# Performance work log

Hardware: AMD Instinct MI355X
Metric: run time of the kernel (lower is better)

The kernel has to match this reference:

```python
import jax, jax.numpy as jnp
import numpy as np

N_NODES = 50000


def rgcn_conv(x, src, dst, edge_type, W, root, bias):
    """PyG RGCNConv: out[i] = x[i] @ root + bias + sum_r mean_{j in N_r(i)} x[j] @ W[r].
    W: [R, F_in, F_out]. Mean aggregation is per-relation (PyG default aggr='mean')."""
    num_rel = W.shape[0]
    n = x.shape[0]
    out = x @ root + bias
    x_src = x[src]  # [E, F_in] gather once
    for r in range(num_rel):  # small fixed relation count
        mask = (edge_type == r)
        msg = jnp.where(mask[:, None], x_src, 0.0) @ W[r]          # [E, F_out]
        s = jax.ops.segment_sum(msg, dst, num_segments=n)           # [N, F_out]
        c = jax.ops.segment_sum(mask.astype(x.dtype), dst, num_segments=n)  # [N]
        out = out + s / jnp.maximum(c, 1.0)[:, None]
    return out


def setup_inputs() -> dict:
    key = jax.random.key(0)
    ks = jax.random.split(key, 10)
    N, E, F_in, F_hid, F_out, R = N_NODES, 800000, 128, 128, 64, 8
    x = jax.random.normal(ks[0], (N, F_in), dtype=jnp.float32)
    edge_index = jax.random.randint(ks[1], (2, E), 0, N, dtype=jnp.int64)
    edge_type = jax.random.randint(ks[2], (E,), 0, R, dtype=jnp.int64)
    s1 = 1.0 / np.sqrt(F_in)
    s2 = 1.0 / np.sqrt(F_hid)
    W1 = jax.random.normal(ks[3], (R, F_in, F_hid), dtype=jnp.float32) * s1
    root1 = jax.random.normal(ks[4], (F_in, F_hid), dtype=jnp.float32) * s1
    b1 = jnp.zeros((F_hid,), dtype=jnp.float32)
    W2 = jax.random.normal(ks[5], (R, F_hid, F_out), dtype=jnp.float32) * s2
    root2 = jax.random.normal(ks[6], (F_hid, F_out), dtype=jnp.float32) * s2
    b2 = jnp.zeros((F_out,), dtype=jnp.float32)
    return {"x": x, "edge_index": edge_index, "edge_type": edge_type,
            "W1": W1, "root1": root1, "b1": b1,
            "W2": W2, "root2": root2, "b2": b2}


def reference(x, edge_index, edge_type, W1, root1, b1, W2, root2, b2):
    src, dst = edge_index[0], edge_index[1]
    h = jax.nn.relu(rgcn_conv(x, src, dst, edge_type, W1, root1, b1))
    out = rgcn_conv(h, src, dst, edge_type, W2, root2, b2)
    return out
```

## Files before the change

kernel.cpp:

```cpp
#include <hip/hip_runtime.h>

#define N_NODES 50000
#define N_EDGES 800000
#define R_REL   8

#define TNBKT   3125
#define TCAP    512
#define SLAB    2048
#define BINBLK  ((N_EDGES + SLAB - 1) / SLAB)

typedef float  f32x4  __attribute__((ext_vector_type(4)));
typedef __bf16 bf16x8 __attribute__((ext_vector_type(8)));

__device__ __forceinline__ unsigned short f2bf(float f) {
    unsigned int u = __float_as_uint(f);
    u = (u + 0x7FFFu + ((u >> 16) & 1u)) >> 16;
    return (unsigned short)u;
}
__device__ __forceinline__ float bflo(unsigned int u) { return __uint_as_float(u << 16); }
__device__ __forceinline__ float bfhi(unsigned int u) { return __uint_as_float(u & 0xFFFF0000u); }

__device__ __forceinline__ void acc16(float* a, uint4 u0, uint4 u1) {
    a[0]  += bflo(u0.x);   a[1]  += bfhi(u0.x);
    a[2]  += bflo(u0.y);   a[3]  += bfhi(u0.y);
    a[4]  += bflo(u0.z);   a[5]  += bfhi(u0.z);
    a[6]  += bflo(u0.w);   a[7]  += bfhi(u0.w);
    a[8]  += bflo(u1.x);   a[9]  += bfhi(u1.x);
    a[10] += bflo(u1.y);   a[11] += bfhi(u1.y);
    a[12] += bflo(u1.z);   a[13] += bfhi(u1.z);
    a[14] += bflo(u1.w);   a[15] += bfhi(u1.w);
}


#define W1_ELEMS (9 * 128 * 128)
#define W2_ELEMS (9 * 64 * 128)
#define N4       (N_NODES * 32)
#define NB_CVT   ((N4 + 255) / 256)
#define NB_PREP  (BINBLK + NB_CVT)

__global__ __launch_bounds__(256) void k_prep(
    const int* __restrict__ src, const int* __restrict__ dst,
    const int* __restrict__ et, int* __restrict__ gcur,
    unsigned* __restrict__ gbin,
    const float* __restrict__ x, unsigned short* __restrict__ xb,
    const float* __restrict__ root1, const float* __restrict__ W1,
    const float* __restrict__ root2, const float* __restrict__ W2,
    unsigned short* __restrict__ Wt1, unsigned short* __restrict__ Wt2)
{
    __shared__ int hist[TNBKT];
    __shared__ int base[TNBKT];
    const int t = threadIdx.x;

    if (blockIdx.x < BINBLK) {
        const int e0 = blockIdx.x * SLAB;
        for (int i = t; i < TNBKT; i += 256) hist[i] = 0;
        __syncthreads();
#pragma unroll
        for (int i = 0; i < SLAB / 256; ++i) {
            int e = e0 + i * 256 + t;
            if (e < N_EDGES) atomicAdd(&hist[dst[e] >> 4], 1);
        }
        __syncthreads();
        for (int i = t; i < TNBKT; i += 256) {
            int h = hist[i];
            base[i] = (h > 0) ? atomicAdd(&gcur[i], h) : 0;
            hist[i] = 0;
        }
        __syncthreads();
#pragma unroll
        for (int i = 0; i < SLAB / 256; ++i) {
            int e = e0 + i * 256 + t;
            if (e < N_EDGES) {
                int d = dst[e];
                int b = d >> 4;
                int sub = atomicAdd(&hist[b], 1);
                int pos = base[b] + sub;
                unsigned rec = ((unsigned)src[e] << 7) | (unsigned)((d & 15) * 8 + et[e]);
                if (pos < TCAP) gbin[(size_t)b * TCAP + pos] = rec;
            }
        }
        return;
    }

    const int idx = (blockIdx.x - BINBLK) * 256 + t;
    if (idx < N4) {
        float4 v = *(const float4*)(x + (size_t)idx * 4);
        ushort4 o;
        o.x = f2bf(v.x); o.y = f2bf(v.y); o.z = f2bf(v.z); o.w = f2bf(v.w);
        *(ushort4*)(xb + (size_t)idx * 4) = o;
    }
    if (idx < W1_ELEMS) {
        int j    = idx & 7;
        int lane = (idx >> 3) & 63;
        int r    = idx >> 9;
        int nb   = r & 7;
        int r2   = r >> 3;
        int kk   = r2 & 3;
        int seg  = r2 >> 2;
        int k = kk * 32 + (lane >> 4) * 8 + j;
        int n = nb * 16 + (lane & 15);
        float v = (seg == 0) ? root1[k * 128 + n] : W1[((seg - 1) * 128 + k) * 128 + n];
        Wt1[idx] = f2bf(v);
    } else if (idx < W1_ELEMS + W2_ELEMS) {
        int i2   = idx - W1_ELEMS;
        int j    = i2 & 7;
        int lane = (i2 >> 3) & 63;
        int r    = i2 >> 9;
        int nb   = r & 3;
        int r2   = r >> 2;
        int kk   = r2 & 3;
        int seg  = r2 >> 2;
        int k = kk * 32 + (lane >> 4) * 8 + j;
        int n = nb * 16 + (lane & 15);
        float v = (seg == 0) ? root2[k * 64 + n] : W2[((seg - 1) * 128 + k) * 64 + n];
        Wt2[i2] = f2bf(v);
    }
}


template <int FOUT, bool RELU, bool OUT_BF16>
__global__ __launch_bounds__(512) void k_fused(
    const unsigned short* __restrict__ xin,
    const unsigned short* __restrict__ WtP,
    const float* __restrict__ bias,
    const int* __restrict__ gcnt,
    const unsigned* __restrict__ gbin,
    unsigned short* __restrict__ outb,
    float* __restrict__ outf)
{
    constexpr int NBt = FOUT / 16;
    __shared__ __align__(16) unsigned short As0[16][136];
    __shared__ __align__(16) unsigned short As[8][16][136];
    __shared__ unsigned short sorted[TCAP + 8];
    __shared__ int dcnt[128];
    __shared__ int kbeg[128];
    __shared__ int kcur[128];

    const int t = threadIdx.x;
    const int node0 = blockIdx.x * 16;

    if (t < 128) { dcnt[t] = 0; kcur[t] = 0; }
    sorted[t] = 0;
    if (t < 8) sorted[TCAP + t] = 0;
    if (t < 128) {
        const int sr = t >> 3;
        const int sp = t & 7;
        const uint4* s4 = (const uint4*)(xin + (size_t)(node0 + sr) * 128 + sp * 16);
        uint4 r0 = s4[0], r1 = s4[1];
        uint4* d = (uint4*)&As0[sr][sp * 16];
        d[0] = r0; d[1] = r1;
    }
    const int nraw = gcnt[blockIdx.x];
    const int n = nraw < TCAP ? nraw : TCAP;
    unsigned rec = 0;
    if (t < n) rec = gbin[(size_t)blockIdx.x * TCAP + t];
    __syncthreads();

    if (t < n) atomicAdd(&dcnt[rec & 127], 1);
    __syncthreads();

    if (t < 64) {
        int d0 = dcnt[2 * t], d1 = dcnt[2 * t + 1];
        int s = d0 + d1;
        int inc = s;
#pragma unroll
        for (int off = 1; off < 64; off <<= 1) {
            int y = __shfl_up(inc, off, 64);
            if (t >= off) inc += y;
        }
        int excl = inc - s;
        kbeg[2 * t]     = excl;
        kbeg[2 * t + 1] = excl + d0;
    }
    __syncthreads();

    if (t < n) {
        int key = rec & 127;
        int pos = atomicAdd(&kcur[key], 1);
        sorted[kbeg[key] + pos] = (unsigned short)(rec >> 7);
    }
    __syncthreads();

    {
        const int key = t >> 2;
        const int q   = t & 3;
        const int rel = key & 7;
        const int nl  = key >> 3;

        const int beg = kbeg[key];
        const int deg = dcnt[key];
        const int end = beg + deg;

        const unsigned short* bx = xin + q * 32;
        float a[32];
#pragma unroll
        for (int i = 0; i < 32; ++i) a[i] = 0.f;

        int j = beg;
        int sA = sorted[j];
        int sB = sorted[j + 1];
        const uint4* pA = (const uint4*)(bx + (size_t)sA * 128);
        const uint4* pB = (const uint4*)(bx + (size_t)sB * 128);
        uint4 A0 = pA[0], A1 = pA[1], A2 = pA[2], A3 = pA[3];
        uint4 B0 = pB[0], B1 = pB[1], B2 = pB[2], B3 = pB[3];

        for (; j + 1 < end; j += 2) {
            int sC = sorted[j + 2];
            int sD = sorted[j + 3];
            const uint4* pC = (const uint4*)(bx + (size_t)sC * 128);
            const uint4* pD = (const uint4*)(bx + (size_t)sD * 128);
            uint4 C0 = pC[0], C1 = pC[1], C2 = pC[2], C3 = pC[3];
            uint4 D0 = pD[0], D1 = pD[1], D2 = pD[2], D3 = pD[3];

            acc16(a, A0, A1);
            acc16(a + 16, A2, A3);
            acc16(a, B0, B1);
            acc16(a + 16, B2, B3);

            A0 = C0; A1 = C1; A2 = C2; A3 = C3;
            B0 = D0; B1 = D1; B2 = D2; B3 = D3;
        }
        if (j < end) {
            acc16(a, A0, A1);
            acc16(a + 16, A2, A3);
        }

        float scl = 1.f / (float)(deg > 1 ? deg : 1);
        unsigned int pk[16];
#pragma unroll
        for (int i = 0; i < 16; ++i)
            pk[i] = (unsigned int)f2bf(a[i * 2] * scl) |
                    ((unsigned int)f2bf(a[i * 2 + 1] * scl) << 16);
        uint4* G = (uint4*)&As[rel][nl][0];
        const int g0 = q * 4;
        G[(g0 + 0) ^ rel] = make_uint4(pk[0],  pk[1],  pk[2],  pk[3]);
        G[(g0 + 1) ^ rel] = make_uint4(pk[4],  pk[5],  pk[6],  pk[7]);
        G[(g0 + 2) ^ rel] = make_uint4(pk[8],  pk[9],  pk[10], pk[11]);
        G[(g0 + 3) ^ rel] = make_uint4(pk[12], pk[13], pk[14], pk[15]);
    }

    __syncthreads();

    const int lane = t & 63;
    const int w = t >> 6;
    if (w >= NBt) return;
    const int quad = lane >> 4;
    const int tc = lane & 15;

    f32x4 acc = (f32x4){0.f, 0.f, 0.f, 0.f};
    const bf16x8* Bp = (const bf16x8*)WtP;

#pragma unroll
    for (int seg = 0; seg < 9; ++seg) {
        const uint4* Ag = (seg == 0) ? (const uint4*)&As0[tc][0]
                                     : (const uint4*)&As[seg - 1][tc][0];
        const int s = (seg == 0) ? 0 : (seg - 1);
#pragma unroll
        for (int kk = 0; kk < 4; ++kk) {
            bf16x8 af = *(const bf16x8*)(Ag + (((kk << 2) + quad) ^ s));
            bf16x8 bf = Bp[((seg * 4 + kk) * NBt + w) * 64 + lane];
            acc = __builtin_amdgcn_mfma_f32_16x16x32_bf16(af, bf, acc, 0, 0, 0);
        }
    }

    const int col = w * 16 + tc;
    const float bs = bias[col];
#pragma unroll
    for (int i = 0; i < 4; ++i) {
        int r = node0 + quad * 4 + i;
        float v = acc[i] + bs;
        if (RELU) v = fmaxf(v, 0.f);
        if (OUT_BF16) outb[(size_t)r * FOUT + col] = f2bf(v);
        else          outf[(size_t)r * FOUT + col] = v;
    }
}


extern "C" void kernel_launch(void* const* d_in, const int* in_sizes, int n_in,
                              void* d_out, int out_size, void* d_ws, size_t ws_size,
                              hipStream_t stream) {
    const float* x     = (const float*)d_in[0];
    const int*   ei    = (const int*)d_in[1];
    const int*   et    = (const int*)d_in[2];
    const float* W1    = (const float*)d_in[3];
    const float* root1 = (const float*)d_in[4];
    const float* b1    = (const float*)d_in[5];
    const float* W2    = (const float*)d_in[6];
    const float* root2 = (const float*)d_in[7];
    const float* b2    = (const float*)d_in[8];
    float* out = (float*)d_out;

    int* ws = (int*)d_ws;
    int* gcur = ws;
    unsigned* gbin = (unsigned*)(gcur + 3200);
    unsigned short* xb  = (unsigned short*)(gbin + (size_t)TNBKT * TCAP);
    unsigned short* hb  = xb + (size_t)N_NODES * 128;
    unsigned short* Wt1 = hb + (size_t)N_NODES * 128;
    unsigned short* Wt2 = Wt1 + W1_ELEMS;

    const int* esrc = ei;
    const int* edst = ei + N_EDGES;

    hipMemsetAsync(gcur, 0, 3200 * sizeof(int), stream);
    k_prep<<<NB_PREP, 256, 0, stream>>>(esrc, edst, et, gcur, gbin,
                                        x, xb, root1, W1, root2, W2, Wt1, Wt2);

    const int NT = N_NODES / 16;

    k_fused<128, true,  true ><<<NT, 512, 0, stream>>>(xb, Wt1, b1, gcur, gbin, hb, nullptr);
    k_fused<64,  false, false><<<NT, 512, 0, stream>>>(hb, Wt2, b2, gcur, gbin, nullptr, out);
}
```

Measured before the change: 251.8 us.

## Process five node tiles per block in feature-quarter phases with double-buffered slab

Each block now handles five 16-node tiles, sorting all their edge bins up front, then loops over four 32-feature quarters. Within each quarter it gathers neighbor means per tile into a small double-buffered LDS slab and feeds MFMA accumulators kept in registers per tile. This cuts LDS footprint and register pressure per gather thread (8 floats instead of 32) and lets a quarter of W be reused across five tiles, aiming for better occupancy and latency hiding. In exchange, the grid shrinks from 3125 to 625 blocks, there are more barriers, and each neighbor row is fetched in four separate 16-byte pieces, which may reduce coalescing.

```diff
diff --git a/kernel.cpp b/kernel.cpp
--- a/kernel.cpp
+++ b/kernel.cpp
@@ -9,6 +9,10 @@
 #define SLAB    2048
 #define BINBLK  ((N_EDGES + SLAB - 1) / SLAB)
 
+#define NBLK    625
+#define TPB     5
+#define SEGST   648
+
 typedef float  f32x4  __attribute__((ext_vector_type(4)));
 typedef __bf16 bf16x8 __attribute__((ext_vector_type(8)));
 
@@ -20,15 +24,11 @@
 __device__ __forceinline__ float bflo(unsigned int u) { return __uint_as_float(u << 16); }
 __device__ __forceinline__ float bfhi(unsigned int u) { return __uint_as_float(u & 0xFFFF0000u); }
 
-__device__ __forceinline__ void acc16(float* a, uint4 u0, uint4 u1) {
-    a[0]  += bflo(u0.x);   a[1]  += bfhi(u0.x);
-    a[2]  += bflo(u0.y);   a[3]  += bfhi(u0.y);
-    a[4]  += bflo(u0.z);   a[5]  += bfhi(u0.z);
-    a[6]  += bflo(u0.w);   a[7]  += bfhi(u0.w);
-    a[8]  += bflo(u1.x);   a[9]  += bfhi(u1.x);
-    a[10] += bflo(u1.y);   a[11] += bfhi(u1.y);
-    a[12] += bflo(u1.z);   a[13] += bfhi(u1.z);
-    a[14] += bflo(u1.w);   a[15] += bfhi(u1.w);
+__device__ __forceinline__ void acc8(float* a, uint4 u) {
+    a[0] += bflo(u.x); a[1] += bfhi(u.x);
+    a[2] += bflo(u.y); a[3] += bfhi(u.y);
+    a[4] += bflo(u.z); a[5] += bfhi(u.z);
+    a[6] += bflo(u.w); a[7] += bfhi(u.w);
 }
 
 
@@ -119,7 +119,7 @@
 
 
 template <int FOUT, bool RELU, bool OUT_BF16>
-__global__ __launch_bounds__(512) void k_fused(
+__global__ __launch_bounds__(512) void k_phase(
     const unsigned short* __restrict__ xin,
     const unsigned short* __restrict__ WtP,
     const float* __restrict__ bias,
@@ -129,149 +129,147 @@
     float* __restrict__ outf)
 {
     constexpr int NBt = FOUT / 16;
-    __shared__ __align__(16) unsigned short As0[16][136];
-    __shared__ __align__(16) unsigned short As[8][16][136];
-    __shared__ unsigned short sorted[TCAP + 8];
+    __shared__ unsigned short sorted[TPB][TCAP];
+    __shared__ unsigned short degb[TPB][128];
+    __shared__ unsigned short begb[TPB][128];
+    __shared__ __align__(16) unsigned short slab[2 * SEGST * 9];
     __shared__ int dcnt[128];
-    __shared__ int kbeg[128];
     __shared__ int kcur[128];
 
     const int t = threadIdx.x;
-    const int node0 = blockIdx.x * 16;
-
-    if (t < 128) { dcnt[t] = 0; kcur[t] = 0; }
-    sorted[t] = 0;
-    if (t < 8) sorted[TCAP + t] = 0;
-    if (t < 128) {
-        const int sr = t >> 3;
-        const int sp = t & 7;
-        const uint4* s4 = (const uint4*)(xin + (size_t)(node0 + sr) * 128 + sp * 16);
-        uint4 r0 = s4[0], r1 = s4[1];
-        uint4* d = (uint4*)&As0[sr][sp * 16];
-        d[0] = r0; d[1] = r1;
-    }
-    const int nraw = gcnt[blockIdx.x];
-    const int n = nraw < TCAP ? nraw : TCAP;
-    unsigned rec = 0;
-    if (t < n) rec = gbin[(size_t)blockIdx.x * TCAP + t];
-    __syncthreads();
-
-    if (t < n) atomicAdd(&dcnt[rec & 127], 1);
-    __syncthreads();
-
-    if (t < 64) {
-        int d0 = dcnt[2 * t], d1 = dcnt[2 * t + 1];
-        int s = d0 + d1;
-        int inc = s;
-#pragma unroll
-        for (int off = 1; off < 64; off <<= 1) {
-            int y = __shfl_up(inc, off, 64);
-            if (t >= off) inc += y;
-        }
-        int excl = inc - s;
-        kbeg[2 * t]     = excl;
-        kbeg[2 * t + 1] = excl + d0;
-    }
-    __syncthreads();
-
-    if (t < n) {
-        int key = rec & 127;
-        int pos = atomicAdd(&kcur[key], 1);
-        sorted[kbeg[key] + pos] = (unsigned short)(rec >> 7);
-    }
-    __syncthreads();
-
-    {
-        const int key = t >> 2;
-        const int q   = t & 3;
-        const int rel = key & 7;
-        const int nl  = key >> 3;
-
-        const int beg = kbeg[key];
-        const int deg = dcnt[key];
-        const int end = beg + deg;
-
-        const unsigned short* bx = xin + q * 32;
-        float a[32];
-#pragma unroll
-        for (int i = 0; i < 32; ++i) a[i] = 0.f;
-
-        int j = beg;
-        int sA = sorted[j];
-        int sB = sorted[j + 1];
-        const uint4* pA = (const uint4*)(bx + (size_t)sA * 128);
-        const uint4* pB = (const uint4*)(bx + (size_t)sB * 128);
-        uint4 A0 = pA[0], A1 = pA[1], A2 = pA[2], A3 = pA[3];
-        uint4 B0 = pB[0], B1 = pB[1], B2 = pB[2], B3 = pB[3];
-
-        for (; j + 1 < end; j += 2) {
-            int sC = sorted[j + 2];
-            int sD = sorted[j + 3];
-            const uint4* pC = (const uint4*)(bx + (size_t)sC * 128);
-            const uint4* pD = (const uint4*)(bx + (size_t)sD * 128);
-            uint4 C0 = pC[0], C1 = pC[1], C2 = pC[2], C3 = pC[3];
-            uint4 D0 = pD[0], D1 = pD[1], D2 = pD[2], D3 = pD[3];
-
-            acc16(a, A0, A1);
-            acc16(a + 16, A2, A3);
-            acc16(a, B0, B1);
-            acc16(a + 16, B2, B3);
-
-            A0 = C0; A1 = C1; A2 = C2; A3 = C3;
-            B0 = D0; B1 = D1; B2 = D2; B3 = D3;
-        }
-        if (j < end) {
-            acc16(a, A0, A1);
-            acc16(a + 16, A2, A3);
-        }
-
-        float scl = 1.f / (float)(deg > 1 ? deg : 1);
-        unsigned int pk[16];
-#pragma unroll
-        for (int i = 0; i < 16; ++i)
-            pk[i] = (unsigned int)f2bf(a[i * 2] * scl) |
-                    ((unsigned int)f2bf(a[i * 2 + 1] * scl) << 16);
-        uint4* G = (uint4*)&As[rel][nl][0];
-        const int g0 = q * 4;
-        G[(g0 + 0) ^ rel] = make_uint4(pk[0],  pk[1],  pk[2],  pk[3]);
-        G[(g0 + 1) ^ rel] = make_uint4(pk[4],  pk[5],  pk[6],  pk[7]);
-        G[(g0 + 2) ^ rel] = make_uint4(pk[8],  pk[9],  pk[10], pk[11]);
-        G[(g0 + 3) ^ rel] = make_uint4(pk[12], pk[13], pk[14], pk[15]);
-    }
-
-    __syncthreads();
+    const int tile0 = blockIdx.x * TPB;
+
+    for (int ti = 0; ti < TPB; ++ti) {
+        if (t < 128) { dcnt[t] = 0; kcur[t] = 0; }
+        __syncthreads();
+        const int tile = tile0 + ti;
+        const int nraw = gcnt[tile];
+        const int n = nraw < TCAP ? nraw : TCAP;
+        unsigned rec = 0;
+        if (t < n) {
+            rec = gbin[(size_t)tile * TCAP + t];
+            atomicAdd(&dcnt[rec & 127], 1);
+        }
+        __syncthreads();
+        if (t < 64) {
+            int d0 = dcnt[2 * t], d1 = dcnt[2 * t + 1];
+            int s = d0 + d1, inc = s;
+#pragma unroll
+            for (int off = 1; off < 64; off <<= 1) {
+                int y = __shfl_up(inc, off, 64);
+                if (t >= off) inc += y;
+            }
+            int excl = inc - s;
+            begb[ti][2 * t]     = (unsigned short)excl;
+            begb[ti][2 * t + 1] = (unsigned short)(excl + d0);
+            degb[ti][2 * t]     = (unsigned short)d0;
+            degb[ti][2 * t + 1] = (unsigned short)d1;
+        }
+        __syncthreads();
+        if (t < n) {
+            int key = rec & 127;
+            int pos = atomicAdd(&kcur[key], 1);
+            sorted[ti][(int)begb[ti][key] + pos] = (unsigned short)(rec >> 7);
+        }
+        __syncthreads();
+    }
 
     const int lane = t & 63;
-    const int w = t >> 6;
-    if (w >= NBt) return;
+    const int w    = t >> 6;
     const int quad = lane >> 4;
-    const int tc = lane & 15;
-
-    f32x4 acc = (f32x4){0.f, 0.f, 0.f, 0.f};
-    const bf16x8* Bp = (const bf16x8*)WtP;
-
-#pragma unroll
-    for (int seg = 0; seg < 9; ++seg) {
-        const uint4* Ag = (seg == 0) ? (const uint4*)&As0[tc][0]
-                                     : (const uint4*)&As[seg - 1][tc][0];
-        const int s = (seg == 0) ? 0 : (seg - 1);
-#pragma unroll
-        for (int kk = 0; kk < 4; ++kk) {
-            bf16x8 af = *(const bf16x8*)(Ag + (((kk << 2) + quad) ^ s));
-            bf16x8 bf = Bp[((seg * 4 + kk) * NBt + w) * 64 + lane];
-            acc = __builtin_amdgcn_mfma_f32_16x16x32_bf16(af, bf, acc, 0, 0, 0);
-        }
-    }
-
-    const int col = w * 16 + tc;
-    const float bs = bias[col];
-#pragma unroll
-    for (int i = 0; i < 4; ++i) {
-        int r = node0 + quad * 4 + i;
-        float v = acc[i] + bs;
-        if (RELU) v = fmaxf(v, 0.f);
-        if (OUT_BF16) outb[(size_t)r * FOUT + col] = f2bf(v);
-        else          outf[(size_t)r * FOUT + col] = v;
+    const int tc   = lane & 15;
+    const int sub  = t & 3;
+    const int key  = t >> 2;
+    const int rel  = key & 7;
+    const int nl   = key >> 3;
+
+    f32x4 acc[TPB];
+#pragma unroll
+    for (int i = 0; i < TPB; ++i) acc[i] = (f32x4){0.f, 0.f, 0.f, 0.f};
+
+    int buf = 0;
+    for (int q = 0; q < 4; ++q) {
+#pragma unroll
+        for (int ti = 0; ti < TPB; ++ti) {
+            unsigned short* sl = slab + buf * (SEGST * 9);
+            const int node0 = (tile0 + ti) * 16;
+
+            if (t < 64) {
+                int row = t >> 2, piece = t & 3;
+                uint4 v = *(const uint4*)(xin + (size_t)(node0 + row) * 128 + q * 32 + piece * 8);
+                *(uint4*)(sl + row * 40 + piece * 8) = v;
+            }
+
+            {
+                const int deg = degb[ti][key];
+                const int beg = begb[ti][key];
+                const int end = beg + deg;
+                const unsigned short* bx = xin + q * 32 + sub * 8;
+                const unsigned short* srt = sorted[ti];
+                float a[8];
+#pragma unroll
+                for (int i = 0; i < 8; ++i) a[i] = 0.f;
+                int j = beg;
+                for (; j + 3 < end; j += 4) {
+                    int s0 = srt[j], s1 = srt[j + 1], s2 = srt[j + 2], s3 = srt[j + 3];
+                    uint4 v0 = *(const uint4*)(bx + (size_t)s0 * 128);
+                    uint4 v1 = *(const uint4*)(bx + (size_t)s1 * 128);
+                    uint4 v2 = *(const uint4*)(bx + (size_t)s2 * 128);
+                    uint4 v3 = *(const uint4*)(bx + (size_t)s3 * 128);
+                    acc8(a, v0); acc8(a, v1); acc8(a, v2); acc8(a, v3);
+                }
+                if (j + 1 < end) {
+                    int s0 = srt[j], s1 = srt[j + 1];
+                    uint4 v0 = *(const uint4*)(bx + (size_t)s0 * 128);
+                    uint4 v1 = *(const uint4*)(bx + (size_t)s1 * 128);
+                    acc8(a, v0); acc8(a, v1);
+                    j += 2;
+                }
+                if (j < end) {
+                    uint4 v0 = *(const uint4*)(bx + (size_t)srt[j] * 128);
+                    acc8(a, v0);
+                }
+                float scl = 1.f / (float)(deg > 1 ? deg : 1);
+                unsigned pk0 = (unsigned)f2bf(a[0] * scl) | ((unsigned)f2bf(a[1] * scl) << 16);
+                unsigned pk1 = (unsigned)f2bf(a[2] * scl) | ((unsigned)f2bf(a[3] * scl) << 16);
+                unsigned pk2 = (unsigned)f2bf(a[4] * scl) | ((unsigned)f2bf(a[5] * scl) << 16);
+                unsigned pk3 = (unsigned)f2bf(a[6] * scl) | ((unsigned)f2bf(a[7] * scl) << 16);
+                *(uint4*)(sl + (1 + rel) * SEGST + nl * 40 + sub * 8) =
+                    make_uint4(pk0, pk1, pk2, pk3);
+            }
+
+            __syncthreads();
+
+            if (w < NBt) {
+                const bf16x8* Bp = (const bf16x8*)WtP;
+                f32x4 av = acc[ti];
+#pragma unroll
+                for (int seg = 0; seg < 9; ++seg) {
+                    bf16x8 af = *(const bf16x8*)(sl + seg * SEGST + tc * 40 + quad * 8);
+                    bf16x8 bf = Bp[((seg * 4 + q) * NBt + w) * 64 + lane];
+                    av = __builtin_amdgcn_mfma_f32_16x16x32_bf16(af, bf, av, 0, 0, 0);
+                }
+                acc[ti] = av;
+            }
+            buf ^= 1;
+        }
+    }
+
+    if (w < NBt) {
+        const int col = w * 16 + tc;
+        const float bs = bias[col];
+#pragma unroll
+        for (int ti = 0; ti < TPB; ++ti) {
+            const int node0 = (tile0 + ti) * 16;
+#pragma unroll
+            for (int i = 0; i < 4; ++i) {
+                int r = node0 + quad * 4 + i;
+                float v = acc[ti][i] + bs;
+                if (RELU) v = fmaxf(v, 0.f);
+                if (OUT_BF16) outb[(size_t)r * FOUT + col] = f2bf(v);
+                else          outf[(size_t)r * FOUT + col] = v;
+            }
+        }
     }
 }
 
@@ -305,8 +303,6 @@
     k_prep<<<NB_PREP, 256, 0, stream>>>(esrc, edst, et, gcur, gbin,
                                         x, xb, root1, W1, root2, W2, Wt1, Wt2);
 
-    const int NT = N_NODES / 16;
-
-    k_fused<128, true,  true ><<<NT, 512, 0, stream>>>(xb, Wt1, b1, gcur, gbin, hb, nullptr);
-    k_fused<64,  false, false><<<NT, 512, 0, stream>>>(hb, Wt2, b2, gcur, gbin, nullptr, out);
-}
+    k_phase<128, true,  true ><<<NBLK, 512, 0, stream>>>(xb, Wt1, b1, gcur, gbin, hb, nullptr);
+    k_phase<64,  false, false><<<NBLK, 512, 0, stream>>>(hb, Wt2, b2, gcur, gbin, nullptr, out);
+}
```

Result: slower. 331.6 us (+31.7%).
